# Optimization experiments

Measured on AMD Instinct MI355X. Metric: run time of the kernel, lower is better.

Reference implementation:

```python
import jax, jax.numpy as jnp
import numpy as np


def _nearest(x, h, w):
    # torch F.interpolate(mode='nearest'): src_idx = floor(dst_idx * in/out)
    Hi, Wi = x.shape[-2], x.shape[-1]
    ri = (jnp.arange(h) * Hi) // h
    ci = (jnp.arange(w) * Wi) // w
    return jnp.take(jnp.take(x, ri, axis=-2), ci, axis=-1)


def _conv2d(x, wgt, bias):
    y = jax.lax.conv_general_dilated(x, wgt, (1, 1), 'SAME',
                                     dimension_numbers=('NCHW', 'OIHW', 'NCHW'))
    return y + bias.reshape(1, -1, 1, 1)


def setup_inputs() -> dict:
    key = jax.random.key(0)
    ks = jax.random.split(key, 6)
    b, c, ref_n, h, w = 1, 128, 4, 64, 64
    Hv, Wv = 256, 256
    return {
        'feats_t': jax.random.normal(ks[0], (b, c, h, w), jnp.float32),
        'feats_ref': jax.random.normal(ks[1], (b, c, ref_n, h, w), jnp.float32),
        'v_t': jax.random.uniform(ks[2], (b, 1, Hv, Wv), dtype=jnp.float32),
        'v_ref': jax.random.uniform(ks[3], (b, 1, ref_n, Hv, Wv), dtype=jnp.float32),
        'conv1_w': jax.random.normal(ks[4], (1, 1, 3, 3), jnp.float32) * 0.1,
        'conv1_b': jnp.zeros((1,), jnp.float32),
        'conv2_w': jax.random.normal(ks[5], (1, 1, 3, 3), jnp.float32) * 0.1,
        'conv2_b': jnp.zeros((1,), jnp.float32),
    }


def reference(feats_t, feats_ref, v_t, v_ref, conv1_w, conv1_b, conv2_w, conv2_b):
    b, c, ref_n, h, w = feats_ref.shape
    # nearest-resize visibility masks to feature resolution
    vt = _nearest(v_t, h, w)                      # (b, 1, h, w)
    vr = _nearest(v_ref, h, w)                    # (b, 1, ref_n, h, w)
    ft = feats_t * vt                             # (b, c, h, w)
    fr = feats_ref * vr                           # (b, c, ref_n, h, w)
    # cost volume: corr[b,r,q,k] = sum_c ft[b,c,q] * fr[b,c,r,k]
    corr = jnp.einsum('bcq,bcrk->brqk',
                      ft.reshape(b, c, h * w),
                      fr.reshape(b, c, ref_n, h * w))
    corr = corr.reshape(b, ref_n, h, w, h, w)
    # separable 4D conv: 3x3 over (h_ref, w_ref), then 3x3 over (h_t, w_t)
    x = _conv2d(corr.reshape(b * ref_n * h * w, 1, h, w), conv1_w, conv1_b)
    x = x.reshape(b, ref_n, h, w, h, w).transpose(0, 1, 4, 5, 2, 3)
    x = _conv2d(x.reshape(b * ref_n * h * w, 1, h, w), conv2_w, conv2_b)
    corr = x.reshape(b, ref_n, h, w, h, w).transpose(0, 1, 4, 5, 2, 3)
    # softmax3d: joint softmax over (ref_n, h_ref, w_ref) per query location
    m = jnp.max(corr, axis=(1, 4, 5), keepdims=True)
    e = jnp.exp(corr - m)
    corr = e / jnp.sum(e, axis=(1, 4, 5), keepdims=True)
    # weighted aggregation: out[b,c,q] = sum_{r,k} fr[b,c,r,k] * corr[b,r,q,k]
    out = jnp.einsum('bcrk,brqk->bcq',
                     fr.reshape(b, c, ref_n, h * w),
                     corr.reshape(b, ref_n, h * w, h * w))
    return out.reshape(b, c, h, w)
```

## Files before the change

### kernel.cpp

```cpp
#include <hip/hip_runtime.h>
#include <stdint.h>
#include <math.h>

typedef short bf16x8 __attribute__((ext_vector_type(8)));
typedef float f32x16 __attribute__((ext_vector_type(16)));
typedef unsigned int uint4v __attribute__((ext_vector_type(4)));

#define GAS __attribute__((address_space(1)))
#define LAS __attribute__((address_space(3)))

#define CDIM 128
#define NQ   4096
#define NK   16384
#define QT   128
#define KTILE 32
#define NBUF 3
#define LOG2E 1.4426950408889634f

__device__ __forceinline__ unsigned short f2bf(float f) {
    unsigned int u = __builtin_bit_cast(unsigned int, f);
    u = (u + 0x7fffu + ((u >> 16) & 1u)) >> 16;
    return (unsigned short)u;
}

__device__ __forceinline__ void gload_lds16(const void* g, void* l) {
    __builtin_amdgcn_global_load_lds((const GAS unsigned int*)g, (LAS unsigned int*)l, 16, 0, 0);
}

__device__ __forceinline__ unsigned cvtpk(float a, float b) {
    unsigned r;
    asm("v_cvt_pk_bf16_f32 %0, %1, %2" : "=v"(r) : "v"(a), "v"(b));
    return r;
}

__device__ __forceinline__ void swap32(unsigned& a, unsigned& b) {
    asm("v_permlane32_swap_b32 %0, %1" : "+v"(a), "+v"(b));
}

__global__ void prep_q_kernel(const float* __restrict__ feats_t,
                              const float* __restrict__ v_t,
                              const float* __restrict__ w2,
                              unsigned int* __restrict__ Q32) {
    int idx = blockIdx.x * 256 + threadIdx.x;
    int q = idx & 4095, cp = idx >> 12;
    int y = q >> 6, x = q & 63;
    const float* fb0 = feats_t + (size_t)(cp * 2) * 4096;
    const float* fb1 = fb0 + 4096;
    float wv[9];
#pragma unroll
    for (int i = 0; i < 9; ++i) wv[i] = w2[i];
    float acc0 = 0.f, acc1 = 0.f;
#pragma unroll
    for (int u = 0; u < 3; ++u) {
        int yy = y + u - 1;
        if ((unsigned)yy >= 64u) continue;
#pragma unroll
        for (int v = 0; v < 3; ++v) {
            int xx = x + v - 1;
            if ((unsigned)xx >= 64u) continue;
            float m = wv[u * 3 + v] * v_t[yy * 1024 + xx * 4];
            acc0 += m * fb0[yy * 64 + xx];
            acc1 += m * fb1[yy * 64 + xx];
        }
    }
    Q32[(size_t)q * 64 + cp] =
        (unsigned)f2bf(acc0 * LOG2E) | ((unsigned)f2bf(acc1 * LOG2E) << 16);
}

__global__ void prep_p_kernel(const float* __restrict__ feats_ref,
                              const float* __restrict__ v_ref,
                              float* __restrict__ P,
                              unsigned short* __restrict__ Vt2) {
    int idx = blockIdx.x * 256 + threadIdx.x;
    int c = idx >> 14, rk = idx & 16383;
    int r = rk >> 12, k4 = rk & 4095, ky = k4 >> 6, kx = k4 & 63;
    float v = feats_ref[idx] * v_ref[r * 65536 + ky * 1024 + kx * 4];
    P[idx] = v;
    Vt2[(size_t)(rk >> 5) * 4096 + (((rk >> 3) & 3) * 128 + c) * 8 + (rk & 7)] = f2bf(v);
}

__global__ void prep_k2_kernel(const float* __restrict__ P,
                               const float* __restrict__ w1,
                               unsigned int* __restrict__ K32) {
    int idx = blockIdx.x * 256 + threadIdx.x;
    int rk = idx & 16383, cp2 = idx >> 14;
    int r = rk >> 12, k4 = rk & 4095, ky = k4 >> 6, kx = k4 & 63;
    const float* pb0 = P + (size_t)(cp2 * 2) * NK + r * 4096;
    const float* pb1 = pb0 + NK;
    float wv[9];
#pragma unroll
    for (int i = 0; i < 9; ++i) wv[i] = w1[i];
    float acc0 = 0.f, acc1 = 0.f;
#pragma unroll
    for (int u = 0; u < 3; ++u) {
        int yy = ky + u - 1;
        if ((unsigned)yy >= 64u) continue;
#pragma unroll
        for (int v = 0; v < 3; ++v) {
            int xx = kx + v - 1;
            if ((unsigned)xx >= 64u) continue;
            float w = wv[u * 3 + v];
            acc0 += w * pb0[yy * 64 + xx];
            acc1 += w * pb1[yy * 64 + xx];
        }
    }
    int tile = rk >> 5, rw = rk & 31;
    K32[(size_t)tile * 2048 + ((cp2 >> 2) * 32 + rw) * 4 + (cp2 & 3)] =
        (unsigned)f2bf(acc0) | ((unsigned)f2bf(acc1) << 16);
}

template<int KS>
__launch_bounds__(256, 2)
__global__ void attn_kernel(const unsigned short* __restrict__ Qg,
                            const unsigned short* __restrict__ Kt,
                            const unsigned short* __restrict__ Vt2,
                            float* __restrict__ Opart,
                            float* __restrict__ lpart) {
    constexpr int NITER = (NK / KS) / KTILE;
    __shared__ __align__(16) unsigned short KV[NBUF][2][4096];

    const int tid = threadIdx.x;
    const int wid = tid >> 6;
    const int lane = tid & 63;
    const int l31 = lane & 31;
    const int lh = lane >> 5;
    const int ks = blockIdx.x & (KS - 1);
    const int qt = blockIdx.x / KS;
    const int q0 = qt * QT + wid * 32;
    const int tile0 = ks * NITER;

    bf16x8 qf[8];
#pragma unroll
    for (int s = 0; s < 8; ++s)
        qf[s] = *(const bf16x8*)(Qg + (size_t)(q0 + l31) * CDIM + s * 16 + lh * 8);

    f32x16 accO[4];
#pragma unroll
    for (int u = 0; u < 4; ++u)
#pragma unroll
        for (int r = 0; r < 16; ++r) accO[u][r] = 0.f;
    float l_acc = 0.f;

#define STAGE(nb, tg)                                                             \
    do {                                                                          \
        _Pragma("unroll") for (int j = 0; j < 2; ++j) {                           \
            int mb = (wid * 2 + j) * 64;                                          \
            gload_lds16(Kt + (size_t)(tg) * 4096 + (mb + lane) * 8,               \
                        &KV[(nb)][0][mb * 8]);                                    \
            gload_lds16(Vt2 + (size_t)(tg) * 4096 + (mb + lane) * 8,              \
                        &KV[(nb)][1][mb * 8]);                                    \
        }                                                                         \
    } while (0)

    STAGE(0, tile0);
    STAGE(1, tile0 + 1);
    int bc = 0;

#pragma unroll 1
    for (int it = 0; it < NITER; ++it) {
        if (it + 1 < NITER)
            asm volatile("s_waitcnt vmcnt(4)" ::: "memory");
        else
            asm volatile("s_waitcnt vmcnt(0)" ::: "memory");
        __syncthreads();
        if (it + 2 < NITER) {
            int bs = bc + 2; if (bs >= NBUF) bs -= NBUF;
            STAGE(bs, tile0 + it + 2);
        }

        f32x16 S;
#pragma unroll
        for (int r = 0; r < 16; ++r) S[r] = 0.f;
        __builtin_amdgcn_s_setprio(1);
#pragma unroll
        for (int s = 0; s < 8; ++s) {
            bf16x8 kf = *(const bf16x8*)(&KV[bc][0][((s * 2 + lh) * 32 + l31) * 8]);
            S = __builtin_amdgcn_mfma_f32_32x32x16_bf16(kf, qf[s], S, 0, 0, 0);
        }
        __builtin_amdgcn_s_setprio(0);
#pragma unroll
        for (int r = 0; r < 16; ++r) { S[r] = exp2f(S[r]); l_acc += S[r]; }
        unsigned w0 = cvtpk(S[0], S[1]),   w1 = cvtpk(S[2], S[3]);
        unsigned w2 = cvtpk(S[4], S[5]),   w3 = cvtpk(S[6], S[7]);
        unsigned w4 = cvtpk(S[8], S[9]),   w5 = cvtpk(S[10], S[11]);
        unsigned w6 = cvtpk(S[12], S[13]), w7 = cvtpk(S[14], S[15]);
        swap32(w0, w2);
        swap32(w1, w3);
        swap32(w4, w6);
        swap32(w5, w7);
        bf16x8 pbA = __builtin_bit_cast(bf16x8, (uint4v){w0, w1, w2, w3});
        bf16x8 pbB = __builtin_bit_cast(bf16x8, (uint4v){w4, w5, w6, w7});
        __builtin_amdgcn_s_setprio(1);
#pragma unroll
        for (int u = 0; u < 4; ++u) {
            bf16x8 vfa = *(const bf16x8*)(&KV[bc][1][((lh) * 128 + u * 32 + l31) * 8]);
            accO[u] = __builtin_amdgcn_mfma_f32_32x32x16_bf16(vfa, pbA, accO[u], 0, 0, 0);
            bf16x8 vfb = *(const bf16x8*)(&KV[bc][1][((2 + lh) * 128 + u * 32 + l31) * 8]);
            accO[u] = __builtin_amdgcn_mfma_f32_32x32x16_bf16(vfb, pbB, accO[u], 0, 0, 0);
        }
        __builtin_amdgcn_s_setprio(0);
        bc = bc + 1; if (bc >= NBUF) bc -= NBUF;
    }
#undef STAGE

    l_acc += __shfl_xor(l_acc, 32);
    if (lane < 32) lpart[ks * NQ + q0 + l31] = l_acc;
#pragma unroll
    for (int u = 0; u < 4; ++u)
#pragma unroll
        for (int r = 0; r < 16; ++r) {
            int c = u * 32 + (r & 3) + 8 * (r >> 2) + 4 * lh;
            Opart[((size_t)(ks * CDIM + c)) * NQ + q0 + l31] = accO[u][r];
        }
}

template<int KS>
__global__ void reduce_kernel(const float* __restrict__ Opart,
                              const float* __restrict__ lpart,
                              float* __restrict__ out) {
    int i = blockIdx.x * 256 + threadIdx.x;
    int c = i >> 12, q = i & 4095;
    float den = 0.f, o = 0.f;
#pragma unroll
    for (int s = 0; s < KS; ++s) {
        den += lpart[s * NQ + q];
        o += Opart[((size_t)(s * CDIM + c)) * NQ + q];
    }
    out[(size_t)c * NQ + q] = o / den;
}

extern "C" void kernel_launch(void* const* d_in, const int* in_sizes, int n_in,
                              void* d_out, int out_size, void* d_ws, size_t ws_size,
                              hipStream_t stream) {
    (void)in_sizes; (void)n_in; (void)out_size;
    const float* feats_t   = (const float*)d_in[0];
    const float* feats_ref = (const float*)d_in[1];
    const float* v_t       = (const float*)d_in[2];
    const float* v_ref     = (const float*)d_in[3];
    const float* w1        = (const float*)d_in[4];
    const float* w2        = (const float*)d_in[6];
    float* out = (float*)d_out;

    const size_t opart_off = (size_t)(9u << 20);
    const size_t per_split = (size_t)NQ * CDIM * 4;
    const size_t need16 = opart_off + 16 * per_split + 16 * NQ * 4;
    const size_t need8  = opart_off + 8  * per_split + 8  * NQ * 4;
    if (ws_size < need8) return;

    char* ws = (char*)d_ws;
    unsigned int*   Q   = (unsigned int*)(ws);
    unsigned short* Kt  = (unsigned short*)(ws + (size_t)(1u << 20));
    unsigned short* Vt2 = (unsigned short*)(ws + (size_t)(5u << 20));
    float* Opart = (float*)(ws + opart_off);
    float* P     = Opart;

    hipLaunchKernelGGL(prep_q_kernel, dim3(1024), dim3(256), 0, stream, feats_t, v_t, w2, Q);
    hipLaunchKernelGGL(prep_p_kernel, dim3(8192), dim3(256), 0, stream, feats_ref, v_ref, P, Vt2);
    hipLaunchKernelGGL(prep_k2_kernel, dim3(4096), dim3(256), 0, stream, P, w1, (unsigned int*)Kt);

    if (ws_size >= need16) {
        float* lpart = (float*)(ws + opart_off + 16 * per_split);
        hipLaunchKernelGGL(HIP_KERNEL_NAME(attn_kernel<16>), dim3((NQ / QT) * 16), dim3(256), 0,
                           stream, (const unsigned short*)Q, Kt, Vt2, Opart, lpart);
        hipLaunchKernelGGL(HIP_KERNEL_NAME(reduce_kernel<16>), dim3(2048), dim3(256), 0,
                           stream, Opart, lpart, out);
    } else {
        float* lpart = (float*)(ws + opart_off + 8 * per_split);
        hipLaunchKernelGGL(HIP_KERNEL_NAME(attn_kernel<8>), dim3((NQ / QT) * 8), dim3(256), 0,
                           stream, (const unsigned short*)Q, Kt, Vt2, Opart, lpart);
        hipLaunchKernelGGL(HIP_KERNEL_NAME(reduce_kernel<8>), dim3(2048), dim3(256), 0,
                           stream, Opart, lpart, out);
    }
}
```

Measured before the change: 79.76 us.

## Double K tile to 64 keys with double-buffered LDS staging

Raises the attention key tile from 32 to 64 and switches from a triple-buffered to a double-buffered LDS ring. The K and V layouts written by the prep kernels change to match. Each iteration now runs two independent score MFMA chains and twice the PV MFMAs, so per-tile barrier and wait overhead is spread over more work and the MFMA pipe gets more independent work. In exchange there are two barriers per iteration, prefetch runs only one tile ahead, and register pressure rises, which may hurt occupancy at 2 blocks per CU.

```diff
diff --git a/kernel.cpp b/kernel.cpp
--- a/kernel.cpp
+++ b/kernel.cpp
@@ -13,8 +13,7 @@
 #define NQ   4096
 #define NK   16384
 #define QT   128
-#define KTILE 32
-#define NBUF 3
+#define KTILE 64
 #define LOG2E 1.4426950408889634f
 
 __device__ __forceinline__ unsigned short f2bf(float f) {
@@ -76,7 +75,7 @@
     int r = rk >> 12, k4 = rk & 4095, ky = k4 >> 6, kx = k4 & 63;
     float v = feats_ref[idx] * v_ref[r * 65536 + ky * 1024 + kx * 4];
     P[idx] = v;
-    Vt2[(size_t)(rk >> 5) * 4096 + (((rk >> 3) & 3) * 128 + c) * 8 + (rk & 7)] = f2bf(v);
+    Vt2[(size_t)(rk >> 6) * 8192 + (((rk >> 3) & 7) * 128 + c) * 8 + (rk & 7)] = f2bf(v);
 }
 
 __global__ void prep_k2_kernel(const float* __restrict__ P,
@@ -104,8 +103,8 @@
             acc1 += w * pb1[yy * 64 + xx];
         }
     }
-    int tile = rk >> 5, rw = rk & 31;
-    K32[(size_t)tile * 2048 + ((cp2 >> 2) * 32 + rw) * 4 + (cp2 & 3)] =
+    int tile = rk >> 6, rw = rk & 63;
+    K32[(size_t)tile * 4096 + ((cp2 >> 2) * 64 + rw) * 4 + (cp2 & 3)] =
         (unsigned)f2bf(acc0) | ((unsigned)f2bf(acc1) << 16);
 }
 
@@ -117,7 +116,7 @@
                             float* __restrict__ Opart,
                             float* __restrict__ lpart) {
     constexpr int NITER = (NK / KS) / KTILE;
-    __shared__ __align__(16) unsigned short KV[NBUF][2][4096];
+    __shared__ __align__(16) unsigned short KV[2][2][8192];
 
     const int tid = threadIdx.x;
     const int wid = tid >> 6;
@@ -143,63 +142,76 @@
 
 #define STAGE(nb, tg)                                                             \
     do {                                                                          \
-        _Pragma("unroll") for (int j = 0; j < 2; ++j) {                           \
-            int mb = (wid * 2 + j) * 64;                                          \
-            gload_lds16(Kt + (size_t)(tg) * 4096 + (mb + lane) * 8,               \
+        _Pragma("unroll") for (int j = 0; j < 4; ++j) {                           \
+            int mb = (wid * 4 + j) * 64;                                          \
+            gload_lds16(Kt + (size_t)(tg) * 8192 + (mb + lane) * 8,               \
                         &KV[(nb)][0][mb * 8]);                                    \
-            gload_lds16(Vt2 + (size_t)(tg) * 4096 + (mb + lane) * 8,              \
+            gload_lds16(Vt2 + (size_t)(tg) * 8192 + (mb + lane) * 8,              \
                         &KV[(nb)][1][mb * 8]);                                    \
         }                                                                         \
     } while (0)
 
     STAGE(0, tile0);
-    STAGE(1, tile0 + 1);
-    int bc = 0;
 
 #pragma unroll 1
     for (int it = 0; it < NITER; ++it) {
-        if (it + 1 < NITER)
-            asm volatile("s_waitcnt vmcnt(4)" ::: "memory");
-        else
+        const int bc = it & 1;
+        __syncthreads();
+        if (it + 1 < NITER) {
+            STAGE(bc ^ 1, tile0 + it + 1);
+            asm volatile("s_waitcnt vmcnt(8)" ::: "memory");
+        } else {
             asm volatile("s_waitcnt vmcnt(0)" ::: "memory");
+        }
         __syncthreads();
-        if (it + 2 < NITER) {
-            int bs = bc + 2; if (bs >= NBUF) bs -= NBUF;
-            STAGE(bs, tile0 + it + 2);
-        }
-
-        f32x16 S;
-#pragma unroll
-        for (int r = 0; r < 16; ++r) S[r] = 0.f;
+
+        f32x16 S0, S1;
+#pragma unroll
+        for (int r = 0; r < 16; ++r) { S0[r] = 0.f; S1[r] = 0.f; }
         __builtin_amdgcn_s_setprio(1);
 #pragma unroll
         for (int s = 0; s < 8; ++s) {
-            bf16x8 kf = *(const bf16x8*)(&KV[bc][0][((s * 2 + lh) * 32 + l31) * 8]);
-            S = __builtin_amdgcn_mfma_f32_32x32x16_bf16(kf, qf[s], S, 0, 0, 0);
+            bf16x8 kf0 = *(const bf16x8*)(&KV[bc][0][((s * 2 + lh) * 64 + l31) * 8]);
+            S0 = __builtin_amdgcn_mfma_f32_32x32x16_bf16(kf0, qf[s], S0, 0, 0, 0);
+            bf16x8 kf1 = *(const bf16x8*)(&KV[bc][0][((s * 2 + lh) * 64 + 32 + l31) * 8]);
+            S1 = __builtin_amdgcn_mfma_f32_32x32x16_bf16(kf1, qf[s], S1, 0, 0, 0);
         }
         __builtin_amdgcn_s_setprio(0);
-#pragma unroll
-        for (int r = 0; r < 16; ++r) { S[r] = exp2f(S[r]); l_acc += S[r]; }
-        unsigned w0 = cvtpk(S[0], S[1]),   w1 = cvtpk(S[2], S[3]);
-        unsigned w2 = cvtpk(S[4], S[5]),   w3 = cvtpk(S[6], S[7]);
-        unsigned w4 = cvtpk(S[8], S[9]),   w5 = cvtpk(S[10], S[11]);
-        unsigned w6 = cvtpk(S[12], S[13]), w7 = cvtpk(S[14], S[15]);
-        swap32(w0, w2);
-        swap32(w1, w3);
-        swap32(w4, w6);
-        swap32(w5, w7);
-        bf16x8 pbA = __builtin_bit_cast(bf16x8, (uint4v){w0, w1, w2, w3});
-        bf16x8 pbB = __builtin_bit_cast(bf16x8, (uint4v){w4, w5, w6, w7});
+
+        float e0[16], e1[16];
+#pragma unroll
+        for (int r = 0; r < 16; ++r) { e0[r] = exp2f(S0[r]); l_acc += e0[r]; }
+#pragma unroll
+        for (int r = 0; r < 16; ++r) { e1[r] = exp2f(S1[r]); l_acc += e1[r]; }
+
+        unsigned a0 = cvtpk(e0[0], e0[1]),   a1 = cvtpk(e0[2], e0[3]);
+        unsigned a2 = cvtpk(e0[4], e0[5]),   a3 = cvtpk(e0[6], e0[7]);
+        unsigned a4 = cvtpk(e0[8], e0[9]),   a5 = cvtpk(e0[10], e0[11]);
+        unsigned a6 = cvtpk(e0[12], e0[13]), a7 = cvtpk(e0[14], e0[15]);
+        swap32(a0, a2); swap32(a1, a3); swap32(a4, a6); swap32(a5, a7);
+        unsigned b0 = cvtpk(e1[0], e1[1]),   b1 = cvtpk(e1[2], e1[3]);
+        unsigned b2 = cvtpk(e1[4], e1[5]),   b3 = cvtpk(e1[6], e1[7]);
+        unsigned b4 = cvtpk(e1[8], e1[9]),   b5 = cvtpk(e1[10], e1[11]);
+        unsigned b6 = cvtpk(e1[12], e1[13]), b7 = cvtpk(e1[14], e1[15]);
+        swap32(b0, b2); swap32(b1, b3); swap32(b4, b6); swap32(b5, b7);
+        bf16x8 pA0 = __builtin_bit_cast(bf16x8, (uint4v){a0, a1, a2, a3});
+        bf16x8 pB0 = __builtin_bit_cast(bf16x8, (uint4v){a4, a5, a6, a7});
+        bf16x8 pA1 = __builtin_bit_cast(bf16x8, (uint4v){b0, b1, b2, b3});
+        bf16x8 pB1 = __builtin_bit_cast(bf16x8, (uint4v){b4, b5, b6, b7});
+
         __builtin_amdgcn_s_setprio(1);
 #pragma unroll
         for (int u = 0; u < 4; ++u) {
-            bf16x8 vfa = *(const bf16x8*)(&KV[bc][1][((lh) * 128 + u * 32 + l31) * 8]);
-            accO[u] = __builtin_amdgcn_mfma_f32_32x32x16_bf16(vfa, pbA, accO[u], 0, 0, 0);
-            bf16x8 vfb = *(const bf16x8*)(&KV[bc][1][((2 + lh) * 128 + u * 32 + l31) * 8]);
-            accO[u] = __builtin_amdgcn_mfma_f32_32x32x16_bf16(vfb, pbB, accO[u], 0, 0, 0);
+            bf16x8 v0a = *(const bf16x8*)(&KV[bc][1][((lh) * 128 + u * 32 + l31) * 8]);
+            accO[u] = __builtin_amdgcn_mfma_f32_32x32x16_bf16(v0a, pA0, accO[u], 0, 0, 0);
+            bf16x8 v0b = *(const bf16x8*)(&KV[bc][1][((2 + lh) * 128 + u * 32 + l31) * 8]);
+            accO[u] = __builtin_amdgcn_mfma_f32_32x32x16_bf16(v0b, pB0, accO[u], 0, 0, 0);
+            bf16x8 v1a = *(const bf16x8*)(&KV[bc][1][((4 + lh) * 128 + u * 32 + l31) * 8]);
+            accO[u] = __builtin_amdgcn_mfma_f32_32x32x16_bf16(v1a, pA1, accO[u], 0, 0, 0);
+            bf16x8 v1b = *(const bf16x8*)(&KV[bc][1][((6 + lh) * 128 + u * 32 + l31) * 8]);
+            accO[u] = __builtin_amdgcn_mfma_f32_32x32x16_bf16(v1b, pB1, accO[u], 0, 0, 0);
         }
         __builtin_amdgcn_s_setprio(0);
-        bc = bc + 1; if (bc >= NBUF) bc -= NBUF;
     }
 #undef STAGE
 
```

Measured after the change: 78.47 us. About the same (-1.6%).

## Shrink attention query tile to 64 with double-buffered K/V staging

Applied to the files above, without the earlier changes.

Halves the query tile per block (128 threads, two waves) and replaces the three-buffer prefetch pipeline with a two-buffer scheme that issues the next tile's loads after a barrier. The LOG2E pre-scaling of Q is removed in favour of __expf in the softmax, and the row-sum uses a tree reduction. Smaller blocks allow more blocks per CU, but each K/V tile is loaded and reused by half as many queries, and the extra barrier per iteration shortens the prefetch distance.

```diff
diff --git a/kernel.cpp b/kernel.cpp
--- a/kernel.cpp
+++ b/kernel.cpp
@@ -12,10 +12,8 @@
 #define CDIM 128
 #define NQ   4096
 #define NK   16384
-#define QT   128
+#define QT   64
 #define KTILE 32
-#define NBUF 3
-#define LOG2E 1.4426950408889634f
 
 __device__ __forceinline__ unsigned short f2bf(float f) {
     unsigned int u = __builtin_bit_cast(unsigned int, f);
@@ -63,8 +61,7 @@
             acc1 += m * fb1[yy * 64 + xx];
         }
     }
-    Q32[(size_t)q * 64 + cp] =
-        (unsigned)f2bf(acc0 * LOG2E) | ((unsigned)f2bf(acc1 * LOG2E) << 16);
+    Q32[(size_t)q * 64 + cp] = (unsigned)f2bf(acc0) | ((unsigned)f2bf(acc1) << 16);
 }
 
 __global__ void prep_p_kernel(const float* __restrict__ feats_ref,
@@ -110,14 +107,14 @@
 }
 
 template<int KS>
-__launch_bounds__(256, 2)
+__launch_bounds__(128, 2)
 __global__ void attn_kernel(const unsigned short* __restrict__ Qg,
                             const unsigned short* __restrict__ Kt,
                             const unsigned short* __restrict__ Vt2,
                             float* __restrict__ Opart,
                             float* __restrict__ lpart) {
     constexpr int NITER = (NK / KS) / KTILE;
-    __shared__ __align__(16) unsigned short KV[NBUF][2][4096];
+    __shared__ __align__(16) unsigned short KV[2][2][4096];
 
     const int tid = threadIdx.x;
     const int wid = tid >> 6;
@@ -143,8 +140,8 @@
 
 #define STAGE(nb, tg)                                                             \
     do {                                                                          \
-        _Pragma("unroll") for (int j = 0; j < 2; ++j) {                           \
-            int mb = (wid * 2 + j) * 64;                                          \
+        _Pragma("unroll") for (int j = 0; j < 4; ++j) {                           \
+            int mb = (wid * 4 + j) * 64;                                          \
             gload_lds16(Kt + (size_t)(tg) * 4096 + (mb + lane) * 8,               \
                         &KV[(nb)][0][mb * 8]);                                    \
             gload_lds16(Vt2 + (size_t)(tg) * 4096 + (mb + lane) * 8,              \
@@ -153,20 +150,18 @@
     } while (0)
 
     STAGE(0, tile0);
-    STAGE(1, tile0 + 1);
-    int bc = 0;
 
 #pragma unroll 1
     for (int it = 0; it < NITER; ++it) {
-        if (it + 1 < NITER)
-            asm volatile("s_waitcnt vmcnt(4)" ::: "memory");
-        else
+        const int bc = it & 1;
+        __syncthreads();
+        if (it + 1 < NITER) {
+            STAGE(bc ^ 1, tile0 + it + 1);
+            asm volatile("s_waitcnt vmcnt(8)" ::: "memory");
+        } else {
             asm volatile("s_waitcnt vmcnt(0)" ::: "memory");
+        }
         __syncthreads();
-        if (it + 2 < NITER) {
-            int bs = bc + 2; if (bs >= NBUF) bs -= NBUF;
-            STAGE(bs, tile0 + it + 2);
-        }
 
         f32x16 S;
 #pragma unroll
@@ -178,28 +173,34 @@
             S = __builtin_amdgcn_mfma_f32_32x32x16_bf16(kf, qf[s], S, 0, 0, 0);
         }
         __builtin_amdgcn_s_setprio(0);
-#pragma unroll
-        for (int r = 0; r < 16; ++r) { S[r] = exp2f(S[r]); l_acc += S[r]; }
-        unsigned w0 = cvtpk(S[0], S[1]),   w1 = cvtpk(S[2], S[3]);
-        unsigned w2 = cvtpk(S[4], S[5]),   w3 = cvtpk(S[6], S[7]);
-        unsigned w4 = cvtpk(S[8], S[9]),   w5 = cvtpk(S[10], S[11]);
-        unsigned w6 = cvtpk(S[12], S[13]), w7 = cvtpk(S[14], S[15]);
-        swap32(w0, w2);
-        swap32(w1, w3);
-        swap32(w4, w6);
-        swap32(w5, w7);
-        bf16x8 pbA = __builtin_bit_cast(bf16x8, (uint4v){w0, w1, w2, w3});
-        bf16x8 pbB = __builtin_bit_cast(bf16x8, (uint4v){w4, w5, w6, w7});
+
+        float e[16];
+#pragma unroll
+        for (int r = 0; r < 16; ++r) e[r] = __expf(S[r]);
+        {
+            float t0 = (e[0] + e[1]) + (e[2] + e[3]);
+            float t1 = (e[4] + e[5]) + (e[6] + e[7]);
+            float t2 = (e[8] + e[9]) + (e[10] + e[11]);
+            float t3 = (e[12] + e[13]) + (e[14] + e[15]);
+            l_acc += (t0 + t1) + (t2 + t3);
+        }
+        unsigned a0 = cvtpk(e[0], e[1]),   a1 = cvtpk(e[2], e[3]);
+        unsigned a2 = cvtpk(e[4], e[5]),   a3 = cvtpk(e[6], e[7]);
+        unsigned a4 = cvtpk(e[8], e[9]),   a5 = cvtpk(e[10], e[11]);
+        unsigned a6 = cvtpk(e[12], e[13]), a7 = cvtpk(e[14], e[15]);
+        swap32(a0, a2); swap32(a1, a3); swap32(a4, a6); swap32(a5, a7);
+        bf16x8 pA = __builtin_bit_cast(bf16x8, (uint4v){a0, a1, a2, a3});
+        bf16x8 pB = __builtin_bit_cast(bf16x8, (uint4v){a4, a5, a6, a7});
+
         __builtin_amdgcn_s_setprio(1);
 #pragma unroll
         for (int u = 0; u < 4; ++u) {
             bf16x8 vfa = *(const bf16x8*)(&KV[bc][1][((lh) * 128 + u * 32 + l31) * 8]);
-            accO[u] = __builtin_amdgcn_mfma_f32_32x32x16_bf16(vfa, pbA, accO[u], 0, 0, 0);
+            accO[u] = __builtin_amdgcn_mfma_f32_32x32x16_bf16(vfa, pA, accO[u], 0, 0, 0);
             bf16x8 vfb = *(const bf16x8*)(&KV[bc][1][((2 + lh) * 128 + u * 32 + l31) * 8]);
-            accO[u] = __builtin_amdgcn_mfma_f32_32x32x16_bf16(vfb, pbB, accO[u], 0, 0, 0);
+            accO[u] = __builtin_amdgcn_mfma_f32_32x32x16_bf16(vfb, pB, accO[u], 0, 0, 0);
         }
         __builtin_amdgcn_s_setprio(0);
-        bc = bc + 1; if (bc >= NBUF) bc -= NBUF;
     }
 #undef STAGE
 
@@ -260,13 +261,13 @@
 
     if (ws_size >= need16) {
         float* lpart = (float*)(ws + opart_off + 16 * per_split);
-        hipLaunchKernelGGL(HIP_KERNEL_NAME(attn_kernel<16>), dim3((NQ / QT) * 16), dim3(256), 0,
+        hipLaunchKernelGGL(HIP_KERNEL_NAME(attn_kernel<16>), dim3((NQ / QT) * 16), dim3(128), 0,
                            stream, (const unsigned short*)Q, Kt, Vt2, Opart, lpart);
         hipLaunchKernelGGL(HIP_KERNEL_NAME(reduce_kernel<16>), dim3(2048), dim3(256), 0,
                            stream, Opart, lpart, out);
     } else {
         float* lpart = (float*)(ws + opart_off + 8 * per_split);
-        hipLaunchKernelGGL(HIP_KERNEL_NAME(attn_kernel<8>), dim3((NQ / QT) * 8), dim3(256), 0,
+        hipLaunchKernelGGL(HIP_KERNEL_NAME(attn_kernel<8>), dim3((NQ / QT) * 8), dim3(128), 0,
                            stream, (const unsigned short*)Q, Kt, Vt2, Opart, lpart);
         hipLaunchKernelGGL(HIP_KERNEL_NAME(reduce_kernel<8>), dim3(2048), dim3(256), 0,
                            stream, Opart, lpart, out);
```

Measured after the change: 83.67 us. +4.9%, slower.
